# Kernel optimization log

Measured on AMD Instinct MI355X. Metric: run time of the kernel, lower is better.

The kernel has to match this reference:

```python
import jax, jax.numpy as jnp
import numpy as np

EPS = 1e-6
N_HEADS = 128
QK_NOPE = 128
QK_ROPE = 64
KV_RANK = 512

def rmsnorm(x, gamma):
    var = jnp.mean(jnp.square(x), axis=-1, keepdims=True)
    return x * jax.lax.rsqrt(var + EPS) * gamma

def apply_rope(x, cos, sin):
    # x: [..., D], cos/sin broadcastable to x; rotate-half convention
    x1, x2 = jnp.split(x, 2, axis=-1)
    rot = jnp.concatenate([-x2, x1], axis=-1)
    return x * cos + rot * sin

def setup_inputs() -> dict:
    key = jax.random.key(0)
    ks = jax.random.split(key, 6)
    T, H = 4096, 7168
    inp = {
        "token_x": jax.random.normal(ks[0], (T, H), jnp.float32),
        "wq_a": jax.random.normal(ks[1], (H, 1536), jnp.float32) * 0.02,
        "wq_b": jax.random.normal(ks[2], (1536, N_HEADS * (QK_NOPE + QK_ROPE)), jnp.float32) * 0.02,
        "wkv": jax.random.normal(ks[3], (H, KV_RANK + QK_ROPE), jnp.float32) * 0.02,
        "rope_cos": jax.random.uniform(ks[4], (T, QK_ROPE), jnp.float32, -1.0, 1.0),
        "rope_sin": jax.random.uniform(ks[5], (T, QK_ROPE), jnp.float32, -1.0, 1.0),
        "gamma_cq": jnp.ones((1536,), jnp.float32),
        "gamma_ckv": jnp.ones((KV_RANK,), jnp.float32),
    }
    return inp

def reference(token_x, wq_a, wq_b, wkv, rope_cos, rope_sin, gamma_cq, gamma_ckv):
    T = token_x.shape[0]
    # Query path: down-proj -> RMSNorm -> up-proj -> split -> RoPE on rope part
    cq = rmsnorm(token_x @ wq_a, gamma_cq)                    # [T, 1536]
    q = (cq @ wq_b).reshape(T, N_HEADS, QK_NOPE + QK_ROPE)    # [T, H, 192]
    q_nope, q_rope = q[..., :QK_NOPE], q[..., QK_NOPE:]
    q_rope = apply_rope(q_rope, rope_cos[:, None, :], rope_sin[:, None, :])
    query = jnp.concatenate([q_nope, q_rope], axis=-1)        # [T, H, 192]
    # KV path: joint down-proj -> split latent / rope-key -> RMSNorm + RoPE
    kv = token_x @ wkv                                        # [T, 576]
    ckv = rmsnorm(kv[:, :KV_RANK], gamma_ckv)                 # [T, 512]
    k_rope = apply_rope(kv[:, KV_RANK:], rope_cos, rope_sin)  # [T, 64]
    # Pack outputs into a single array: [T, H*192 + 512 + 64]
    return jnp.concatenate([query.reshape(T, -1), ckv, k_rope], axis=-1)
```

## Files before the change

kernel.cpp:

```cpp
#include <hip/hip_runtime.h>


typedef __attribute__((ext_vector_type(8))) __bf16 bf16x8;
typedef __attribute__((ext_vector_type(4))) float f32x4;

#define OUT_LD 25152

__device__ __forceinline__ unsigned short f2bf(float f) {
  union { float f; unsigned u; } v; v.f = f;
  unsigned r = v.u + 0x7FFFu + ((v.u >> 16) & 1u);
  return (unsigned short)(r >> 16);
}

__device__ __forceinline__ void gload16(const void* g, void* l) {
  __builtin_amdgcn_global_load_lds(
      (__attribute__((address_space(1))) void*)(void*)g,
      (__attribute__((address_space(3))) void*)l, 16, 0, 0);
}

__global__ void cvt_bf16(const float* __restrict__ in, unsigned short* __restrict__ out) {
  size_t i = (size_t)blockIdx.x * 256 + threadIdx.x;
  float4 f = ((const float4*)in)[i];
  ushort4 o;
  o.x = f2bf(f.x); o.y = f2bf(f.y); o.z = f2bf(f.z); o.w = f2bf(f.w);
  ((ushort4*)out)[i] = o;
}

__global__ void transpose_cvt(const float* __restrict__ in, unsigned short* __restrict__ out,
                              int K, int N, int Npad) {
  __shared__ float tile[32][33];
  int k0 = blockIdx.x * 32, n0 = blockIdx.y * 32;
  int tx = threadIdx.x, ty = threadIdx.y;
#pragma unroll
  for (int i = 0; i < 4; ++i) {
    int k = k0 + ty + i * 8;
    int n = n0 + tx;
    tile[ty + i * 8][tx] = (n < N) ? in[(size_t)k * N + n] : 0.f;
  }
  __syncthreads();
#pragma unroll
  for (int i = 0; i < 4; ++i) {
    int n = n0 + ty + i * 8;
    int k = k0 + tx;
    if (n < Npad) out[(size_t)n * K + k] = f2bf(tile[tx][ty + i * 8]);
  }
}

__global__ __launch_bounds__(512, 2) void gemm256(
    const unsigned short* __restrict__ A, const unsigned short* __restrict__ B,
    float* __restrict__ C, int K, int ldc, int Mtiles,
    const float* __restrict__ cs, const float* __restrict__ sn, int rope) {
  __shared__ __attribute__((aligned(128))) char lds[131072];
  const int tid = threadIdx.x;
  const int lane = tid & 63;
  const int wr = (tid >> 6) >> 2;
  const int wc = (tid >> 6) & 3;
  const int NT = K >> 6;

  const int nwg = gridDim.x;
  const int per = nwg >> 3;
  const int bid = blockIdx.x;
  const int swz = (bid & 7) * per + (bid >> 3);
  const int bm = swz % Mtiles, bn = swz / Mtiles;

  const int strow = tid >> 3;
  const int stcolb = (((tid & 7) ^ ((tid >> 3) & 7)) << 4);
  const size_t abase = (size_t)(bm * 256) * K;
  const size_t bbase = (size_t)(bn * 256) * K;

  f32x4 acc[2][2][4][2];
  const f32x4 z4 = {0.f, 0.f, 0.f, 0.f};
#pragma unroll
  for (int a = 0; a < 2; ++a)
#pragma unroll
    for (int b = 0; b < 2; ++b)
#pragma unroll
      for (int c = 0; c < 4; ++c)
#pragma unroll
        for (int d = 0; d < 2; ++d) acc[a][b][c][d] = z4;

#define STAGE_A(kt, bsel, u)                                                          \
  do {                                                                                \
    int row_ = (u) * 64 + strow;                                                      \
    gload16((const char*)(A + abase + (size_t)row_ * K + (size_t)(kt) * 64) + stcolb, \
            lds + (bsel) * 65536 + (u) * 8192 + tid * 16);                            \
  } while (0)
#define STAGE_B(kt, bsel, u)                                                          \
  do {                                                                                \
    int lrow_ = (u) * 64 + strow;                                                     \
    int n_ = ((lrow_ >> 5) & 3) * 64 + ((lrow_ >> 7) & 1) * 32 + (lrow_ & 31);        \
    gload16((const char*)(B + bbase + (size_t)n_ * K + (size_t)(kt) * 64) + stcolb,   \
            lds + (bsel) * 65536 + 32768 + (u) * 8192 + tid * 16);                    \
  } while (0)

#define READ_A(dst, QM, LBASE)                                              \
  do {                                                                      \
    _Pragma("unroll") for (int mf = 0; mf < 4; ++mf)                        \
        _Pragma("unroll") for (int ks = 0; ks < 2; ++ks) {                  \
      int row_ = (QM) * 128 + wr * 64 + mf * 16 + (lane & 15);              \
      int in_ = (ks * 64 + ((lane >> 4) << 4)) ^ ((row_ & 7) << 4);         \
      dst[mf][ks] = *(const bf16x8*)((LBASE) + row_ * 128 + in_);           \
    }                                                                       \
  } while (0)
#define READ_B(dst, QN, LBASE)                                              \
  do {                                                                      \
    _Pragma("unroll") for (int nf = 0; nf < 2; ++nf)                        \
        _Pragma("unroll") for (int ks = 0; ks < 2; ++ks) {                  \
      int c_ = wc * 64 + (QN) * 32 + nf * 16 + (lane & 15);                 \
      int rr_ = ((c_ >> 5) & 1) * 128 + ((c_ >> 6) & 3) * 32 + (c_ & 31);   \
      int in_ = (ks * 64 + ((lane >> 4) << 4)) ^ ((rr_ & 7) << 4);          \
      dst[nf][ks] = *(const bf16x8*)((LBASE) + 32768 + rr_ * 128 + in_);    \
    }                                                                       \
  } while (0)
#define MFMA_Q(QM, QN, AF, BB)                                              \
  do {                                                                      \
    __builtin_amdgcn_s_setprio(1);                                          \
    _Pragma("unroll") for (int mf = 0; mf < 4; ++mf)                        \
        _Pragma("unroll") for (int nf = 0; nf < 2; ++nf)                    \
            _Pragma("unroll") for (int ks = 0; ks < 2; ++ks)                \
                acc[QM][QN][mf][nf] = __builtin_amdgcn_mfma_f32_16x16x32_bf16( \
                    AF[mf][ks], BB[nf][ks], acc[QM][QN][mf][nf], 0, 0, 0);  \
    __builtin_amdgcn_s_setprio(0);                                          \
  } while (0)

  STAGE_A(0, 0, 0); STAGE_A(0, 0, 1); STAGE_A(0, 0, 2); STAGE_A(0, 0, 3);
  STAGE_B(0, 0, 0); STAGE_B(0, 0, 1); STAGE_B(0, 0, 2); STAGE_B(0, 0, 3);
  asm volatile("s_waitcnt vmcnt(0)" ::: "memory");
  __builtin_amdgcn_s_barrier();
  __builtin_amdgcn_sched_barrier(0);

  bf16x8 af0[4][2], af1[4][2], bb0[2][2], bb1[2][2];

  for (int t = 0; t < NT; ++t) {
    const int buf = t & 1;
    const int pb = buf ^ 1;
    const char* Lb = lds + buf * 65536;

    if (t + 1 < NT) {
      STAGE_A(t + 1, pb, 0); STAGE_A(t + 1, pb, 1);
      STAGE_A(t + 1, pb, 2); STAGE_A(t + 1, pb, 3);
      STAGE_B(t + 1, pb, 0); STAGE_B(t + 1, pb, 1);
      STAGE_B(t + 1, pb, 2); STAGE_B(t + 1, pb, 3);
    }
    __builtin_amdgcn_sched_barrier(0);

    READ_A(af0, 0, Lb);
    READ_B(bb0, 0, Lb);
    __builtin_amdgcn_sched_barrier(0);
    READ_B(bb1, 1, Lb);
    __builtin_amdgcn_sched_barrier(0);
    READ_A(af1, 1, Lb);
    __builtin_amdgcn_sched_barrier(0);

    asm volatile("s_waitcnt lgkmcnt(12)" ::: "memory");
    __builtin_amdgcn_sched_barrier(0);
    MFMA_Q(0, 0, af0, bb0);

    asm volatile("s_waitcnt lgkmcnt(8)" ::: "memory");
    __builtin_amdgcn_sched_barrier(0);
    MFMA_Q(0, 1, af0, bb1);

    asm volatile("s_waitcnt lgkmcnt(0)" ::: "memory");
    __builtin_amdgcn_sched_barrier(0);
    MFMA_Q(1, 1, af1, bb1);
    MFMA_Q(1, 0, af1, bb0);

    asm volatile("s_waitcnt vmcnt(0)" ::: "memory");
    __builtin_amdgcn_s_barrier();
    __builtin_amdgcn_sched_barrier(0);
  }

  const int colbase = bn * 256 + wc * 64;
  const int rbase = bm * 256 + wr * 64 + ((lane >> 4) << 2);
  const bool isrope = rope && ((colbase % 192) == 128);
  if (isrope) {
#pragma unroll
    for (int qm = 0; qm < 2; ++qm)
#pragma unroll
      for (int mf = 0; mf < 4; ++mf)
#pragma unroll
        for (int nf = 0; nf < 2; ++nf) {
          int i_ = nf * 16 + (lane & 15);
#pragma unroll
          for (int r = 0; r < 4; ++r) {
            int trow = rbase + qm * 128 + mf * 16 + r;
            float c1 = cs[trow * 64 + i_], s1 = sn[trow * 64 + i_];
            float c2 = cs[trow * 64 + 32 + i_], s2 = sn[trow * 64 + 32 + i_];
            float a = acc[qm][0][mf][nf][r], b = acc[qm][1][mf][nf][r];
            C[(size_t)trow * ldc + colbase + i_] = a * c1 - b * s1;
            C[(size_t)trow * ldc + colbase + 32 + i_] = b * c2 + a * s2;
          }
        }
  } else {
#pragma unroll
    for (int qm = 0; qm < 2; ++qm)
#pragma unroll
      for (int qn = 0; qn < 2; ++qn)
#pragma unroll
        for (int mf = 0; mf < 4; ++mf)
#pragma unroll
          for (int nf = 0; nf < 2; ++nf)
#pragma unroll
            for (int r = 0; r < 4; ++r) {
              int trow = rbase + qm * 128 + mf * 16 + r;
              C[(size_t)trow * ldc + colbase + qn * 32 + nf * 16 + (lane & 15)] =
                  acc[qm][qn][mf][nf][r];
            }
  }
#undef MFMA_Q
#undef READ_B
#undef READ_A
#undef STAGE_B
#undef STAGE_A
}

__global__ __launch_bounds__(256, 2) void gemm128(
    const unsigned short* __restrict__ A, const unsigned short* __restrict__ B,
    float* __restrict__ C, int K, int ldc, int Nvalid) {
  __shared__ __attribute__((aligned(128))) unsigned short As[2][128 * 32];
  __shared__ __attribute__((aligned(128))) unsigned short Bs[2][128 * 32];
  const int tid = threadIdx.x;
  const int lane = tid & 63;
  const int wid = tid >> 6;
  const int wr = wid >> 1, wc = wid & 1;
  const int bm = blockIdx.y, bn = blockIdx.x;
  const size_t abase = (size_t)bm * 128 * K;
  const size_t bbase = (size_t)bn * 128 * K;

  f32x4 acc[4][4];
  const f32x4 zero4 = {0.f, 0.f, 0.f, 0.f};
#pragma unroll
  for (int m = 0; m < 4; ++m)
#pragma unroll
    for (int n = 0; n < 4; ++n) acc[m][n] = zero4;

  const int r0 = tid >> 2;
  const int c0 = (tid & 3) * 8;
  const int NT = K >> 5;

#define G128_STAGE(kt, bsel)                                                   \
  do {                                                                         \
    gload16(A + abase + (size_t)r0 * K + (kt) * 32 + c0, As[bsel] + tid * 8);  \
    gload16(A + abase + (size_t)(r0 + 64) * K + (kt) * 32 + c0,                \
            As[bsel] + (256 + tid) * 8);                                       \
    gload16(B + bbase + (size_t)r0 * K + (kt) * 32 + c0, Bs[bsel] + tid * 8);  \
    gload16(B + bbase + (size_t)(r0 + 64) * K + (kt) * 32 + c0,                \
            Bs[bsel] + (256 + tid) * 8);                                       \
  } while (0)

  G128_STAGE(0, 0);
  __syncthreads();

  for (int t = 0; t < NT; ++t) {
    const int buf = t & 1;
    const int pb = buf ^ 1;
    if (t + 1 < NT) G128_STAGE(t + 1, pb);

    bf16x8 af[4], bfr[4];
#pragma unroll
    for (int m = 0; m < 4; ++m)
      af[m] = *(const bf16x8*)(As[buf] + (wr * 64 + m * 16 + (lane & 15)) * 32 + (lane >> 4) * 8);
#pragma unroll
    for (int n = 0; n < 4; ++n)
      bfr[n] = *(const bf16x8*)(Bs[buf] + (wc * 64 + n * 16 + (lane & 15)) * 32 + (lane >> 4) * 8);

    asm volatile("s_waitcnt lgkmcnt(0)" ::: "memory");
    __builtin_amdgcn_sched_barrier(0);
    __builtin_amdgcn_s_setprio(1);
#pragma unroll
    for (int m = 0; m < 4; ++m)
#pragma unroll
      for (int n = 0; n < 4; ++n)
        acc[m][n] = __builtin_amdgcn_mfma_f32_16x16x32_bf16(af[m], bfr[n], acc[m][n], 0, 0, 0);
    __builtin_amdgcn_s_setprio(0);

    __syncthreads();
  }
#undef G128_STAGE

  const int crow0 = bm * 128 + wr * 64 + ((lane >> 4) << 2);
  const int ccol0 = bn * 128 + wc * 64 + (lane & 15);
#pragma unroll
  for (int m = 0; m < 4; ++m) {
#pragma unroll
    for (int n = 0; n < 4; ++n) {
      int col = ccol0 + n * 16;
      if (col < Nvalid) {
#pragma unroll
        for (int r = 0; r < 4; ++r) {
          int row = crow0 + m * 16 + r;
          C[(size_t)row * ldc + col] = acc[m][n][r];
        }
      }
    }
  }
}

__global__ void epi1(const float* __restrict__ raw, const float* __restrict__ gcq,
                     const float* __restrict__ gckv, const float* __restrict__ cs,
                     const float* __restrict__ sn, unsigned short* __restrict__ cqb,
                     float* __restrict__ out) {
  __shared__ float red[4];
  int t = blockIdx.x, tid = threadIdx.x;
  const float* r = raw + (size_t)t * 2176;
  float v[6];
  float ss = 0.f;
#pragma unroll
  for (int i = 0; i < 6; ++i) {
    v[i] = r[tid + i * 256];
    ss += v[i] * v[i];
  }
#pragma unroll
  for (int o = 32; o > 0; o >>= 1) ss += __shfl_xor(ss, o, 64);
  if ((tid & 63) == 0) red[tid >> 6] = ss;
  __syncthreads();
  ss = red[0] + red[1] + red[2] + red[3];
  float sc = rsqrtf(ss * (1.f / 1536.f) + 1e-6f);
#pragma unroll
  for (int i = 0; i < 6; ++i)
    cqb[(size_t)t * 1536 + tid + i * 256] = f2bf(v[i] * sc * gcq[tid + i * 256]);
  float v0 = r[1536 + tid], v1 = r[1792 + tid];
  float s2 = v0 * v0 + v1 * v1;
#pragma unroll
  for (int o = 32; o > 0; o >>= 1) s2 += __shfl_xor(s2, o, 64);
  __syncthreads();
  if ((tid & 63) == 0) red[tid >> 6] = s2;
  __syncthreads();
  s2 = red[0] + red[1] + red[2] + red[3];
  float sck = rsqrtf(s2 * (1.f / 512.f) + 1e-6f);
  float* orow = out + (size_t)t * OUT_LD + 24576;
  orow[tid] = v0 * sck * gckv[tid];
  orow[tid + 256] = v1 * sck * gckv[tid + 256];
  if (tid < 32) {
    float a = r[2048 + tid], b = r[2080 + tid];
    orow[512 + tid] = a * cs[t * 64 + tid] - b * sn[t * 64 + tid];
    orow[544 + tid] = b * cs[t * 64 + 32 + tid] + a * sn[t * 64 + 32 + tid];
  }
}

extern "C" void kernel_launch(void* const* d_in, const int* in_sizes, int n_in,
                              void* d_out, int out_size, void* d_ws, size_t ws_size,
                              hipStream_t stream) {
  const float* token_x = (const float*)d_in[0];
  const float* wq_a = (const float*)d_in[1];
  const float* wq_b = (const float*)d_in[2];
  const float* wkv = (const float*)d_in[3];
  const float* rope_cos = (const float*)d_in[4];
  const float* rope_sin = (const float*)d_in[5];
  const float* gamma_cq = (const float*)d_in[6];
  const float* gamma_ckv = (const float*)d_in[7];
  float* out = (float*)d_out;

  char* ws = (char*)d_ws;
  unsigned short* txb = (unsigned short*)ws;
  unsigned short* wqbT = (unsigned short*)(ws + 58720256);
  unsigned short* Bc = (unsigned short*)(ws + 134217728);
  float* raw = (float*)(ws + 165412864);
  unsigned short* cqb = (unsigned short*)(ws + 201064448);

  cvt_bf16<<<28672, 256, 0, stream>>>(token_x, txb);
  transpose_cvt<<<dim3(7168 / 32, 1536 / 32), dim3(32, 8), 0, stream>>>(wq_a, Bc, 7168, 1536, 1536);
  transpose_cvt<<<dim3(7168 / 32, 640 / 32), dim3(32, 8), 0, stream>>>(
      wkv, Bc + (size_t)1536 * 7168, 7168, 576, 640);
  transpose_cvt<<<dim3(1536 / 32, 24576 / 32), dim3(32, 8), 0, stream>>>(wq_b, wqbT, 1536, 24576, 24576);

  gemm128<<<dim3(17, 32), 256, 0, stream>>>(txb, Bc, raw, 7168, 2176, 2176);

  epi1<<<4096, 256, 0, stream>>>(raw, gamma_cq, gamma_ckv, rope_cos, rope_sin, cqb, out);

  gemm256<<<1536, 512, 0, stream>>>(cqb, wqbT, out, 1536, OUT_LD, 16, rope_cos, rope_sin, 1);
}
```

Baseline: 684.8 us.

## Replace 256x256 up-projection GEMM with 128x256 tile, K=32 steps, higher occupancy

```diff
diff --git a/kernel.cpp b/kernel.cpp
--- a/kernel.cpp
+++ b/kernel.cpp
@@ -46,16 +46,16 @@
   }
 }
 
-__global__ __launch_bounds__(512, 2) void gemm256(
+__global__ __launch_bounds__(512, 4) void gemm_ht(
     const unsigned short* __restrict__ A, const unsigned short* __restrict__ B,
     float* __restrict__ C, int K, int ldc, int Mtiles,
     const float* __restrict__ cs, const float* __restrict__ sn, int rope) {
-  __shared__ __attribute__((aligned(128))) char lds[131072];
+  __shared__ __attribute__((aligned(128))) char lds[49152];
   const int tid = threadIdx.x;
   const int lane = tid & 63;
   const int wr = (tid >> 6) >> 2;
   const int wc = (tid >> 6) & 3;
-  const int NT = K >> 6;
+  const int NT = K >> 5;
 
   const int nwg = gridDim.x;
   const int per = nwg >> 3;
@@ -63,155 +63,102 @@
   const int swz = (bid & 7) * per + (bid >> 3);
   const int bm = swz % Mtiles, bn = swz / Mtiles;
 
-  const int strow = tid >> 3;
-  const int stcolb = (((tid & 7) ^ ((tid >> 3) & 7)) << 4);
-  const size_t abase = (size_t)(bm * 256) * K;
+  const size_t abase = (size_t)(bm * 128) * K;
   const size_t bbase = (size_t)(bn * 256) * K;
 
-  f32x4 acc[2][2][4][2];
+  const int sa = tid >> 3;
+  const int ga = (tid & 7) ^ (sa & 7);
+  const int arow = 2 * sa + (ga >> 2);
+  const int acol = (ga & 3) * 8;
+  const int jb0 = tid, jb1 = 512 + tid;
+  const int sb0 = jb0 >> 3, sb1 = jb1 >> 3;
+  const int gb0 = (jb0 & 7) ^ (sb0 & 7), gb1 = (jb1 & 7) ^ (sb1 & 7);
+  const int brow0 = 2 * sb0 + (gb0 >> 2), brow1 = 2 * sb1 + (gb1 >> 2);
+  const int bcol0 = (gb0 & 3) * 8, bcol1 = (gb1 & 3) * 8;
+
+  f32x4 acc[4][4];
   const f32x4 z4 = {0.f, 0.f, 0.f, 0.f};
 #pragma unroll
-  for (int a = 0; a < 2; ++a)
-#pragma unroll
-    for (int b = 0; b < 2; ++b)
-#pragma unroll
-      for (int c = 0; c < 4; ++c)
-#pragma unroll
-        for (int d = 0; d < 2; ++d) acc[a][b][c][d] = z4;
-
-#define STAGE_A(kt, bsel, u)                                                          \
-  do {                                                                                \
-    int row_ = (u) * 64 + strow;                                                      \
-    gload16((const char*)(A + abase + (size_t)row_ * K + (size_t)(kt) * 64) + stcolb, \
-            lds + (bsel) * 65536 + (u) * 8192 + tid * 16);                            \
+  for (int m = 0; m < 4; ++m)
+#pragma unroll
+    for (int n = 0; n < 4; ++n) acc[m][n] = z4;
+
+#define STAGE(kt, bsel)                                                              \
+  do {                                                                               \
+    char* R_ = lds + (bsel) * 24576;                                                 \
+    gload16(A + abase + (size_t)arow * K + (size_t)(kt) * 32 + acol, R_ + tid * 16); \
+    gload16(B + bbase + (size_t)brow0 * K + (size_t)(kt) * 32 + bcol0,               \
+            R_ + 8192 + jb0 * 16);                                                   \
+    gload16(B + bbase + (size_t)brow1 * K + (size_t)(kt) * 32 + bcol1,               \
+            R_ + 8192 + jb1 * 16);                                                   \
   } while (0)
-#define STAGE_B(kt, bsel, u)                                                          \
-  do {                                                                                \
-    int lrow_ = (u) * 64 + strow;                                                     \
-    int n_ = ((lrow_ >> 5) & 3) * 64 + ((lrow_ >> 7) & 1) * 32 + (lrow_ & 31);        \
-    gload16((const char*)(B + bbase + (size_t)n_ * K + (size_t)(kt) * 64) + stcolb,   \
-            lds + (bsel) * 65536 + 32768 + (u) * 8192 + tid * 16);                    \
-  } while (0)
-
-#define READ_A(dst, QM, LBASE)                                              \
-  do {                                                                      \
-    _Pragma("unroll") for (int mf = 0; mf < 4; ++mf)                        \
-        _Pragma("unroll") for (int ks = 0; ks < 2; ++ks) {                  \
-      int row_ = (QM) * 128 + wr * 64 + mf * 16 + (lane & 15);              \
-      int in_ = (ks * 64 + ((lane >> 4) << 4)) ^ ((row_ & 7) << 4);         \
-      dst[mf][ks] = *(const bf16x8*)((LBASE) + row_ * 128 + in_);           \
-    }                                                                       \
-  } while (0)
-#define READ_B(dst, QN, LBASE)                                              \
-  do {                                                                      \
-    _Pragma("unroll") for (int nf = 0; nf < 2; ++nf)                        \
-        _Pragma("unroll") for (int ks = 0; ks < 2; ++ks) {                  \
-      int c_ = wc * 64 + (QN) * 32 + nf * 16 + (lane & 15);                 \
-      int rr_ = ((c_ >> 5) & 1) * 128 + ((c_ >> 6) & 3) * 32 + (c_ & 31);   \
-      int in_ = (ks * 64 + ((lane >> 4) << 4)) ^ ((rr_ & 7) << 4);          \
-      dst[nf][ks] = *(const bf16x8*)((LBASE) + 32768 + rr_ * 128 + in_);    \
-    }                                                                       \
-  } while (0)
-#define MFMA_Q(QM, QN, AF, BB)                                              \
-  do {                                                                      \
-    __builtin_amdgcn_s_setprio(1);                                          \
-    _Pragma("unroll") for (int mf = 0; mf < 4; ++mf)                        \
-        _Pragma("unroll") for (int nf = 0; nf < 2; ++nf)                    \
-            _Pragma("unroll") for (int ks = 0; ks < 2; ++ks)                \
-                acc[QM][QN][mf][nf] = __builtin_amdgcn_mfma_f32_16x16x32_bf16( \
-                    AF[mf][ks], BB[nf][ks], acc[QM][QN][mf][nf], 0, 0, 0);  \
-    __builtin_amdgcn_s_setprio(0);                                          \
-  } while (0)
-
-  STAGE_A(0, 0, 0); STAGE_A(0, 0, 1); STAGE_A(0, 0, 2); STAGE_A(0, 0, 3);
-  STAGE_B(0, 0, 0); STAGE_B(0, 0, 1); STAGE_B(0, 0, 2); STAGE_B(0, 0, 3);
-  asm volatile("s_waitcnt vmcnt(0)" ::: "memory");
-  __builtin_amdgcn_s_barrier();
-  __builtin_amdgcn_sched_barrier(0);
-
-  bf16x8 af0[4][2], af1[4][2], bb0[2][2], bb1[2][2];
+
+  STAGE(0, 0);
+  __syncthreads();
 
   for (int t = 0; t < NT; ++t) {
     const int buf = t & 1;
-    const int pb = buf ^ 1;
-    const char* Lb = lds + buf * 65536;
-
-    if (t + 1 < NT) {
-      STAGE_A(t + 1, pb, 0); STAGE_A(t + 1, pb, 1);
-      STAGE_A(t + 1, pb, 2); STAGE_A(t + 1, pb, 3);
-      STAGE_B(t + 1, pb, 0); STAGE_B(t + 1, pb, 1);
-      STAGE_B(t + 1, pb, 2); STAGE_B(t + 1, pb, 3);
+    const char* Lb = lds + buf * 24576;
+    if (t + 1 < NT) STAGE(t + 1, buf ^ 1);
+
+    bf16x8 af[4], bb[4];
+#pragma unroll
+    for (int mf = 0; mf < 4; ++mf) {
+      int row_ = wr * 64 + mf * 16 + (lane & 15);
+      int s_ = row_ >> 1;
+      int st_ = (((row_ & 1) * 64 + (lane >> 4) * 16)) ^ ((s_ & 7) << 4);
+      af[mf] = *(const bf16x8*)(Lb + s_ * 128 + st_);
     }
-    __builtin_amdgcn_sched_barrier(0);
-
-    READ_A(af0, 0, Lb);
-    READ_B(bb0, 0, Lb);
-    __builtin_amdgcn_sched_barrier(0);
-    READ_B(bb1, 1, Lb);
-    __builtin_amdgcn_sched_barrier(0);
-    READ_A(af1, 1, Lb);
-    __builtin_amdgcn_sched_barrier(0);
-
-    asm volatile("s_waitcnt lgkmcnt(12)" ::: "memory");
-    __builtin_amdgcn_sched_barrier(0);
-    MFMA_Q(0, 0, af0, bb0);
-
-    asm volatile("s_waitcnt lgkmcnt(8)" ::: "memory");
-    __builtin_amdgcn_sched_barrier(0);
-    MFMA_Q(0, 1, af0, bb1);
-
-    asm volatile("s_waitcnt lgkmcnt(0)" ::: "memory");
-    __builtin_amdgcn_sched_barrier(0);
-    MFMA_Q(1, 1, af1, bb1);
-    MFMA_Q(1, 0, af1, bb0);
-
-    asm volatile("s_waitcnt vmcnt(0)" ::: "memory");
-    __builtin_amdgcn_s_barrier();
-    __builtin_amdgcn_sched_barrier(0);
-  }
+#pragma unroll
+    for (int nf = 0; nf < 4; ++nf) {
+      int n_ = wc * 64 + nf * 16 + (lane & 15);
+      int s_ = n_ >> 1;
+      int st_ = (((n_ & 1) * 64 + (lane >> 4) * 16)) ^ ((s_ & 7) << 4);
+      bb[nf] = *(const bf16x8*)(Lb + 8192 + s_ * 128 + st_);
+    }
+
+    __builtin_amdgcn_s_setprio(1);
+#pragma unroll
+    for (int mf = 0; mf < 4; ++mf)
+#pragma unroll
+      for (int nf = 0; nf < 4; ++nf)
+        acc[mf][nf] = __builtin_amdgcn_mfma_f32_16x16x32_bf16(af[mf], bb[nf], acc[mf][nf], 0, 0, 0);
+    __builtin_amdgcn_s_setprio(0);
+
+    __syncthreads();
+  }
+#undef STAGE
 
   const int colbase = bn * 256 + wc * 64;
-  const int rbase = bm * 256 + wr * 64 + ((lane >> 4) << 2);
+  const int rbase = bm * 128 + wr * 64 + ((lane >> 4) << 2);
   const bool isrope = rope && ((colbase % 192) == 128);
   if (isrope) {
 #pragma unroll
-    for (int qm = 0; qm < 2; ++qm)
-#pragma unroll
-      for (int mf = 0; mf < 4; ++mf)
-#pragma unroll
-        for (int nf = 0; nf < 2; ++nf) {
-          int i_ = nf * 16 + (lane & 15);
-#pragma unroll
-          for (int r = 0; r < 4; ++r) {
-            int trow = rbase + qm * 128 + mf * 16 + r;
-            float c1 = cs[trow * 64 + i_], s1 = sn[trow * 64 + i_];
-            float c2 = cs[trow * 64 + 32 + i_], s2 = sn[trow * 64 + 32 + i_];
-            float a = acc[qm][0][mf][nf][r], b = acc[qm][1][mf][nf][r];
-            C[(size_t)trow * ldc + colbase + i_] = a * c1 - b * s1;
-            C[(size_t)trow * ldc + colbase + 32 + i_] = b * c2 + a * s2;
-          }
+    for (int mf = 0; mf < 4; ++mf)
+#pragma unroll
+      for (int nf = 0; nf < 2; ++nf) {
+        int i_ = nf * 16 + (lane & 15);
+#pragma unroll
+        for (int r = 0; r < 4; ++r) {
+          int trow = rbase + mf * 16 + r;
+          float c1 = cs[trow * 64 + i_], s1 = sn[trow * 64 + i_];
+          float c2 = cs[trow * 64 + 32 + i_], s2 = sn[trow * 64 + 32 + i_];
+          float a = acc[mf][nf][r], b = acc[mf][nf + 2][r];
+          C[(size_t)trow * ldc + colbase + i_] = a * c1 - b * s1;
+          C[(size_t)trow * ldc + colbase + 32 + i_] = b * c2 + a * s2;
         }
+      }
   } else {
 #pragma unroll
-    for (int qm = 0; qm < 2; ++qm)
-#pragma unroll
-      for (int qn = 0; qn < 2; ++qn)
-#pragma unroll
-        for (int mf = 0; mf < 4; ++mf)
-#pragma unroll
-          for (int nf = 0; nf < 2; ++nf)
-#pragma unroll
-            for (int r = 0; r < 4; ++r) {
-              int trow = rbase + qm * 128 + mf * 16 + r;
-              C[(size_t)trow * ldc + colbase + qn * 32 + nf * 16 + (lane & 15)] =
-                  acc[qm][qn][mf][nf][r];
-            }
-  }
-#undef MFMA_Q
-#undef READ_B
-#undef READ_A
-#undef STAGE_B
-#undef STAGE_A
+    for (int mf = 0; mf < 4; ++mf)
+#pragma unroll
+      for (int nf = 0; nf < 4; ++nf)
+#pragma unroll
+        for (int r = 0; r < 4; ++r) {
+          int trow = rbase + mf * 16 + r;
+          C[(size_t)trow * ldc + colbase + nf * 16 + (lane & 15)] = acc[mf][nf][r];
+        }
+  }
 }
 
 __global__ __launch_bounds__(256, 2) void gemm128(
@@ -368,5 +315,5 @@
 
   epi1<<<4096, 256, 0, stream>>>(raw, gamma_cq, gamma_ckv, rope_cos, rope_sin, cqb, out);
 
-  gemm256<<<1536, 512, 0, stream>>>(cqb, wqbT, out, 1536, OUT_LD, 16, rope_cos, rope_sin, 1);
-}
+  gemm_ht<<<3072, 512, 0, stream>>>(cqb, wqbT, out, 1536, OUT_LD, 32, rope_cos, rope_sin, 1);
+}
```

Result: slower. 746.7 us (+9.0%).

## Load B fragments directly from global into registers, halve LDS footprint

Applied to the files above, without the earlier changes.

```diff
diff --git a/kernel.cpp b/kernel.cpp
--- a/kernel.cpp
+++ b/kernel.cpp
@@ -50,7 +50,7 @@
     const unsigned short* __restrict__ A, const unsigned short* __restrict__ B,
     float* __restrict__ C, int K, int ldc, int Mtiles,
     const float* __restrict__ cs, const float* __restrict__ sn, int rope) {
-  __shared__ __attribute__((aligned(128))) char lds[131072];
+  __shared__ __attribute__((aligned(128))) char lds[65536];
   const int tid = threadIdx.x;
   const int lane = tid & 63;
   const int wr = (tid >> 6) >> 2;
@@ -66,7 +66,6 @@
   const int strow = tid >> 3;
   const int stcolb = (((tid & 7) ^ ((tid >> 3) & 7)) << 4);
   const size_t abase = (size_t)(bm * 256) * K;
-  const size_t bbase = (size_t)(bn * 256) * K;
 
   f32x4 acc[2][2][4][2];
   const f32x4 z4 = {0.f, 0.f, 0.f, 0.f};
@@ -83,14 +82,7 @@
   do {                                                                                \
     int row_ = (u) * 64 + strow;                                                      \
     gload16((const char*)(A + abase + (size_t)row_ * K + (size_t)(kt) * 64) + stcolb, \
-            lds + (bsel) * 65536 + (u) * 8192 + tid * 16);                            \
-  } while (0)
-#define STAGE_B(kt, bsel, u)                                                          \
-  do {                                                                                \
-    int lrow_ = (u) * 64 + strow;                                                     \
-    int n_ = ((lrow_ >> 5) & 3) * 64 + ((lrow_ >> 7) & 1) * 32 + (lrow_ & 31);        \
-    gload16((const char*)(B + bbase + (size_t)n_ * K + (size_t)(kt) * 64) + stcolb,   \
-            lds + (bsel) * 65536 + 32768 + (u) * 8192 + tid * 16);                    \
+            lds + (bsel) * 32768 + (u) * 8192 + tid * 16);                            \
   } while (0)
 
 #define READ_A(dst, QM, LBASE)                                              \
@@ -102,16 +94,18 @@
       dst[mf][ks] = *(const bf16x8*)((LBASE) + row_ * 128 + in_);           \
     }                                                                       \
   } while (0)
-#define READ_B(dst, QN, LBASE)                                              \
-  do {                                                                      \
-    _Pragma("unroll") for (int nf = 0; nf < 2; ++nf)                        \
-        _Pragma("unroll") for (int ks = 0; ks < 2; ++ks) {                  \
-      int c_ = wc * 64 + (QN) * 32 + nf * 16 + (lane & 15);                 \
-      int rr_ = ((c_ >> 5) & 1) * 128 + ((c_ >> 6) & 3) * 32 + (c_ & 31);   \
-      int in_ = (ks * 64 + ((lane >> 4) << 4)) ^ ((rr_ & 7) << 4);          \
-      dst[nf][ks] = *(const bf16x8*)((LBASE) + 32768 + rr_ * 128 + in_);    \
-    }                                                                       \
-  } while (0)
+
+#define LOADB(dst, kt)                                                       \
+  do {                                                                       \
+    _Pragma("unroll") for (int qn = 0; qn < 2; ++qn)                         \
+        _Pragma("unroll") for (int nf = 0; nf < 2; ++nf)                     \
+            _Pragma("unroll") for (int ks = 0; ks < 2; ++ks) {               \
+      int n_ = bn * 256 + wc * 64 + qn * 32 + nf * 16 + (lane & 15);         \
+      dst[qn][nf][ks] = *(const bf16x8*)(B + (size_t)n_ * K + (size_t)(kt) * 64 + \
+                                         ks * 32 + ((lane >> 4) << 3));      \
+    }                                                                        \
+  } while (0)
+
 #define MFMA_Q(QM, QN, AF, BB)                                              \
   do {                                                                      \
     __builtin_amdgcn_s_setprio(1);                                          \
@@ -119,56 +113,54 @@
         _Pragma("unroll") for (int nf = 0; nf < 2; ++nf)                    \
             _Pragma("unroll") for (int ks = 0; ks < 2; ++ks)                \
                 acc[QM][QN][mf][nf] = __builtin_amdgcn_mfma_f32_16x16x32_bf16( \
-                    AF[mf][ks], BB[nf][ks], acc[QM][QN][mf][nf], 0, 0, 0);  \
+                    AF[mf][ks], BB[QN][nf][ks], acc[QM][QN][mf][nf], 0, 0, 0); \
     __builtin_amdgcn_s_setprio(0);                                          \
   } while (0)
 
+#define TILE_BODY(T, BUFSEL, BCUR, BNXT)                                    \
+  do {                                                                      \
+    const char* Lb = lds + (BUFSEL) * 32768;                                \
+    if ((T) + 1 < NT) {                                                     \
+      LOADB(BNXT, (T) + 1);                                                 \
+      STAGE_A((T) + 1, (BUFSEL) ^ 1, 0); STAGE_A((T) + 1, (BUFSEL) ^ 1, 1); \
+      STAGE_A((T) + 1, (BUFSEL) ^ 1, 2); STAGE_A((T) + 1, (BUFSEL) ^ 1, 3); \
+    }                                                                       \
+    __builtin_amdgcn_sched_barrier(0);                                      \
+    READ_A(af0, 0, Lb);                                                     \
+    __builtin_amdgcn_sched_barrier(0);                                      \
+    READ_A(af1, 1, Lb);                                                     \
+    __builtin_amdgcn_sched_barrier(0);                                      \
+    asm volatile("s_waitcnt lgkmcnt(8)" ::: "memory");                      \
+    __builtin_amdgcn_sched_barrier(0);                                      \
+    MFMA_Q(0, 0, af0, BCUR);                                                \
+    MFMA_Q(0, 1, af0, BCUR);                                                \
+    asm volatile("s_waitcnt lgkmcnt(0)" ::: "memory");                      \
+    __builtin_amdgcn_sched_barrier(0);                                      \
+    MFMA_Q(1, 1, af1, BCUR);                                                \
+    MFMA_Q(1, 0, af1, BCUR);                                                \
+    asm volatile("s_waitcnt vmcnt(0)" ::: "memory");                        \
+    __builtin_amdgcn_s_barrier();                                           \
+    __builtin_amdgcn_sched_barrier(0);                                      \
+  } while (0)
+
+  bf16x8 af0[4][2], af1[4][2];
+  bf16x8 b0[2][2][2], b1[2][2][2];
   STAGE_A(0, 0, 0); STAGE_A(0, 0, 1); STAGE_A(0, 0, 2); STAGE_A(0, 0, 3);
-  STAGE_B(0, 0, 0); STAGE_B(0, 0, 1); STAGE_B(0, 0, 2); STAGE_B(0, 0, 3);
+  LOADB(b0, 0);
   asm volatile("s_waitcnt vmcnt(0)" ::: "memory");
   __builtin_amdgcn_s_barrier();
   __builtin_amdgcn_sched_barrier(0);
 
-  bf16x8 af0[4][2], af1[4][2], bb0[2][2], bb1[2][2];
-
-  for (int t = 0; t < NT; ++t) {
-    const int buf = t & 1;
-    const int pb = buf ^ 1;
-    const char* Lb = lds + buf * 65536;
-
-    if (t + 1 < NT) {
-      STAGE_A(t + 1, pb, 0); STAGE_A(t + 1, pb, 1);
-      STAGE_A(t + 1, pb, 2); STAGE_A(t + 1, pb, 3);
-      STAGE_B(t + 1, pb, 0); STAGE_B(t + 1, pb, 1);
-      STAGE_B(t + 1, pb, 2); STAGE_B(t + 1, pb, 3);
-    }
-    __builtin_amdgcn_sched_barrier(0);
-
-    READ_A(af0, 0, Lb);
-    READ_B(bb0, 0, Lb);
-    __builtin_amdgcn_sched_barrier(0);
-    READ_B(bb1, 1, Lb);
-    __builtin_amdgcn_sched_barrier(0);
-    READ_A(af1, 1, Lb);
-    __builtin_amdgcn_sched_barrier(0);
-
-    asm volatile("s_waitcnt lgkmcnt(12)" ::: "memory");
-    __builtin_amdgcn_sched_barrier(0);
-    MFMA_Q(0, 0, af0, bb0);
-
-    asm volatile("s_waitcnt lgkmcnt(8)" ::: "memory");
-    __builtin_amdgcn_sched_barrier(0);
-    MFMA_Q(0, 1, af0, bb1);
-
-    asm volatile("s_waitcnt lgkmcnt(0)" ::: "memory");
-    __builtin_amdgcn_sched_barrier(0);
-    MFMA_Q(1, 1, af1, bb1);
-    MFMA_Q(1, 0, af1, bb0);
-
-    asm volatile("s_waitcnt vmcnt(0)" ::: "memory");
-    __builtin_amdgcn_s_barrier();
-    __builtin_amdgcn_sched_barrier(0);
-  }
+  for (int t = 0; t < NT; t += 2) {
+    TILE_BODY(t, (t >> 1) & 1 ? 0 : 0, b0, b1);
+    TILE_BODY(t + 1, 1, b1, b0);
+  }
+
+#undef TILE_BODY
+#undef MFMA_Q
+#undef LOADB
+#undef READ_A
+#undef STAGE_A
 
   const int colbase = bn * 256 + wc * 64;
   const int rbase = bm * 256 + wr * 64 + ((lane >> 4) << 2);
@@ -207,11 +199,6 @@
                   acc[qm][qn][mf][nf][r];
             }
   }
-#undef MFMA_Q
-#undef READ_B
-#undef READ_A
-#undef STAGE_B
-#undef STAGE_A
 }
 
 __global__ __launch_bounds__(256, 2) void gemm128(
```

Measured after the change: 1.609 ms. 135% more time.

## Load B fragments directly from global into registers, halving LDS usage

Applied to the files above, without the earlier changes.

```diff
diff --git a/kernel.cpp b/kernel.cpp
--- a/kernel.cpp
+++ b/kernel.cpp
@@ -50,7 +50,7 @@
     const unsigned short* __restrict__ A, const unsigned short* __restrict__ B,
     float* __restrict__ C, int K, int ldc, int Mtiles,
     const float* __restrict__ cs, const float* __restrict__ sn, int rope) {
-  __shared__ __attribute__((aligned(128))) char lds[131072];
+  __shared__ __attribute__((aligned(128))) char lds[65536];
   const int tid = threadIdx.x;
   const int lane = tid & 63;
   const int wr = (tid >> 6) >> 2;
@@ -66,7 +66,8 @@
   const int strow = tid >> 3;
   const int stcolb = (((tid & 7) ^ ((tid >> 3) & 7)) << 4);
   const size_t abase = (size_t)(bm * 256) * K;
-  const size_t bbase = (size_t)(bn * 256) * K;
+  const unsigned short* Bw = B + (size_t)(bn * 256 + wc * 64 + (lane & 15)) * K +
+                             ((lane >> 4) << 3);
 
   f32x4 acc[2][2][4][2];
   const f32x4 z4 = {0.f, 0.f, 0.f, 0.f};
@@ -83,14 +84,7 @@
   do {                                                                                \
     int row_ = (u) * 64 + strow;                                                      \
     gload16((const char*)(A + abase + (size_t)row_ * K + (size_t)(kt) * 64) + stcolb, \
-            lds + (bsel) * 65536 + (u) * 8192 + tid * 16);                            \
-  } while (0)
-#define STAGE_B(kt, bsel, u)                                                          \
-  do {                                                                                \
-    int lrow_ = (u) * 64 + strow;                                                     \
-    int n_ = ((lrow_ >> 5) & 3) * 64 + ((lrow_ >> 7) & 1) * 32 + (lrow_ & 31);        \
-    gload16((const char*)(B + bbase + (size_t)n_ * K + (size_t)(kt) * 64) + stcolb,   \
-            lds + (bsel) * 65536 + 32768 + (u) * 8192 + tid * 16);                    \
+            lds + (bsel) * 32768 + (u) * 8192 + tid * 16);                            \
   } while (0)
 
 #define READ_A(dst, QM, LBASE)                                              \
@@ -102,16 +96,16 @@
       dst[mf][ks] = *(const bf16x8*)((LBASE) + row_ * 128 + in_);           \
     }                                                                       \
   } while (0)
-#define READ_B(dst, QN, LBASE)                                              \
+
+#define LOADB(dst, kt)                                                      \
   do {                                                                      \
-    _Pragma("unroll") for (int nf = 0; nf < 2; ++nf)                        \
-        _Pragma("unroll") for (int ks = 0; ks < 2; ++ks) {                  \
-      int c_ = wc * 64 + (QN) * 32 + nf * 16 + (lane & 15);                 \
-      int rr_ = ((c_ >> 5) & 1) * 128 + ((c_ >> 6) & 3) * 32 + (c_ & 31);   \
-      int in_ = (ks * 64 + ((lane >> 4) << 4)) ^ ((rr_ & 7) << 4);          \
-      dst[nf][ks] = *(const bf16x8*)((LBASE) + 32768 + rr_ * 128 + in_);    \
-    }                                                                       \
-  } while (0)
+    _Pragma("unroll") for (int qn = 0; qn < 2; ++qn)                        \
+        _Pragma("unroll") for (int nf = 0; nf < 2; ++nf)                    \
+            _Pragma("unroll") for (int ks = 0; ks < 2; ++ks)                \
+                dst[qn][nf][ks] = *(const bf16x8*)(                         \
+                    Bw + (size_t)(qn * 32 + nf * 16) * K + (size_t)(kt) * 64 + ks * 32); \
+  } while (0)
+
 #define MFMA_Q(QM, QN, AF, BB)                                              \
   do {                                                                      \
     __builtin_amdgcn_s_setprio(1);                                          \
@@ -119,56 +113,65 @@
         _Pragma("unroll") for (int nf = 0; nf < 2; ++nf)                    \
             _Pragma("unroll") for (int ks = 0; ks < 2; ++ks)                \
                 acc[QM][QN][mf][nf] = __builtin_amdgcn_mfma_f32_16x16x32_bf16( \
-                    AF[mf][ks], BB[nf][ks], acc[QM][QN][mf][nf], 0, 0, 0);  \
+                    AF[mf][ks], BB[QN][nf][ks], acc[QM][QN][mf][nf], 0, 0, 0); \
     __builtin_amdgcn_s_setprio(0);                                          \
   } while (0)
 
+  bf16x8 af0[4][2], af1[4][2], b[2][2][2];
+
   STAGE_A(0, 0, 0); STAGE_A(0, 0, 1); STAGE_A(0, 0, 2); STAGE_A(0, 0, 3);
-  STAGE_B(0, 0, 0); STAGE_B(0, 0, 1); STAGE_B(0, 0, 2); STAGE_B(0, 0, 3);
+  LOADB(b, 0);
   asm volatile("s_waitcnt vmcnt(0)" ::: "memory");
   __builtin_amdgcn_s_barrier();
   __builtin_amdgcn_sched_barrier(0);
 
-  bf16x8 af0[4][2], af1[4][2], bb0[2][2], bb1[2][2];
-
   for (int t = 0; t < NT; ++t) {
     const int buf = t & 1;
     const int pb = buf ^ 1;
-    const char* Lb = lds + buf * 65536;
-
-    if (t + 1 < NT) {
+    const char* Lb = lds + buf * 32768;
+    const bool more = (t + 1 < NT);
+
+    if (more) {
       STAGE_A(t + 1, pb, 0); STAGE_A(t + 1, pb, 1);
       STAGE_A(t + 1, pb, 2); STAGE_A(t + 1, pb, 3);
-      STAGE_B(t + 1, pb, 0); STAGE_B(t + 1, pb, 1);
-      STAGE_B(t + 1, pb, 2); STAGE_B(t + 1, pb, 3);
     }
     __builtin_amdgcn_sched_barrier(0);
 
+    asm volatile("s_waitcnt vmcnt(4)" ::: "memory");
+    __builtin_amdgcn_sched_barrier(0);
+
     READ_A(af0, 0, Lb);
-    READ_B(bb0, 0, Lb);
-    __builtin_amdgcn_sched_barrier(0);
-    READ_B(bb1, 1, Lb);
     __builtin_amdgcn_sched_barrier(0);
     READ_A(af1, 1, Lb);
     __builtin_amdgcn_sched_barrier(0);
 
-    asm volatile("s_waitcnt lgkmcnt(12)" ::: "memory");
-    __builtin_amdgcn_sched_barrier(0);
-    MFMA_Q(0, 0, af0, bb0);
-
     asm volatile("s_waitcnt lgkmcnt(8)" ::: "memory");
     __builtin_amdgcn_sched_barrier(0);
-    MFMA_Q(0, 1, af0, bb1);
+    MFMA_Q(0, 0, af0, b);
+    MFMA_Q(0, 1, af0, b);
 
     asm volatile("s_waitcnt lgkmcnt(0)" ::: "memory");
     __builtin_amdgcn_sched_barrier(0);
-    MFMA_Q(1, 1, af1, bb1);
-    MFMA_Q(1, 0, af1, bb0);
-
-    asm volatile("s_waitcnt vmcnt(0)" ::: "memory");
+    MFMA_Q(1, 1, af1, b);
+    MFMA_Q(1, 0, af1, b);
+    __builtin_amdgcn_sched_barrier(0);
+
+    if (more) LOADB(b, t + 1);
+    __builtin_amdgcn_sched_barrier(0);
+
+    if (more) {
+      asm volatile("s_waitcnt vmcnt(8)" ::: "memory");
+    } else {
+      asm volatile("s_waitcnt vmcnt(0)" ::: "memory");
+    }
     __builtin_amdgcn_s_barrier();
     __builtin_amdgcn_sched_barrier(0);
   }
+
+#undef MFMA_Q
+#undef LOADB
+#undef READ_A
+#undef STAGE_A
 
   const int colbase = bn * 256 + wc * 64;
   const int rbase = bm * 256 + wr * 64 + ((lane >> 4) << 2);
@@ -186,9 +189,9 @@
             int trow = rbase + qm * 128 + mf * 16 + r;
             float c1 = cs[trow * 64 + i_], s1 = sn[trow * 64 + i_];
             float c2 = cs[trow * 64 + 32 + i_], s2 = sn[trow * 64 + 32 + i_];
-            float a = acc[qm][0][mf][nf][r], b = acc[qm][1][mf][nf][r];
-            C[(size_t)trow * ldc + colbase + i_] = a * c1 - b * s1;
-            C[(size_t)trow * ldc + colbase + 32 + i_] = b * c2 + a * s2;
+            float a = acc[qm][0][mf][nf][r], bv = acc[qm][1][mf][nf][r];
+            C[(size_t)trow * ldc + colbase + i_] = a * c1 - bv * s1;
+            C[(size_t)trow * ldc + colbase + 32 + i_] = bv * c2 + a * s2;
           }
         }
   } else {
@@ -207,11 +210,6 @@
                   acc[qm][qn][mf][nf][r];
             }
   }
-#undef MFMA_Q
-#undef READ_B
-#undef READ_A
-#undef STAGE_B
-#undef STAGE_A
 }
 
 __global__ __launch_bounds__(256, 2) void gemm128(
```

Measured after the change: 837.7 us. 1.22x slower.
